# Optimization experiments

Hardware: AMD Instinct MI355X
Metric: run time of the kernel (lower is better)

## Reference

```python
import jax, jax.numpy as jnp
import numpy as np

NUM_HEADS = 16
LN_EPS = 1e-5

def _layernorm(x, g, b):
    m = jnp.mean(x, axis=-1, keepdims=True)
    v = jnp.var(x, axis=-1, keepdims=True)
    return (x - m) * jax.lax.rsqrt(v + LN_EPS) * g + b

def _mha(xq, xkv, qw, qb, kw, kb, vw, vb, ow, ob, causal):
    B, T, D = xq.shape
    S = xkv.shape[1]
    Hd = D // NUM_HEADS
    q = (xq @ qw + qb).reshape(B, T, NUM_HEADS, Hd)
    k = (xkv @ kw + kb).reshape(B, S, NUM_HEADS, Hd)
    v = (xkv @ vw + vb).reshape(B, S, NUM_HEADS, Hd)
    scores = jnp.einsum('bthd,bshd->bhts', q, k) / np.sqrt(Hd).astype(np.float32)
    if causal:
        mask = jnp.arange(T)[:, None] >= jnp.arange(S)[None, :]
        scores = jnp.where(mask, scores, jnp.float32(-jnp.inf))
    attn = jax.nn.softmax(scores, axis=-1)
    out = jnp.einsum('bhts,bshd->bthd', attn, v).reshape(B, T, D)
    return out @ ow + ob

def setup_inputs() -> dict:
    B, T, S, D, F = 4, 2048, 2048, 1024, 4096
    key = jax.random.key(0)
    ks = jax.random.split(key, 16)
    w = lambda k, shape: jax.random.normal(k, shape, dtype=jnp.float32) * 0.02
    z = lambda n: jnp.zeros((n,), jnp.float32)
    o = lambda n: jnp.ones((n,), jnp.float32)
    return {
        'x': jax.random.normal(ks[0], (B, T, D), dtype=jnp.float32),
        'encoder_output': jax.random.normal(ks[1], (B, S, D), dtype=jnp.float32),
        'sa_qw': w(ks[2], (D, D)), 'sa_qb': z(D),
        'sa_kw': w(ks[3], (D, D)), 'sa_kb': z(D),
        'sa_vw': w(ks[4], (D, D)), 'sa_vb': z(D),
        'sa_ow': w(ks[5], (D, D)), 'sa_ob': z(D),
        'ca_qw': w(ks[6], (D, D)), 'ca_qb': z(D),
        'ca_kw': w(ks[7], (D, D)), 'ca_kb': z(D),
        'ca_vw': w(ks[8], (D, D)), 'ca_vb': z(D),
        'ca_ow': w(ks[9], (D, D)), 'ca_ob': z(D),
        'ff_w1': w(ks[10], (D, F)), 'ff_b1': z(F),
        'ff_w2': w(ks[11], (F, D)), 'ff_b2': z(D),
        'ln1_g': o(D), 'ln1_b': z(D),
        'ln2_g': o(D), 'ln2_b': z(D),
        'ln3_g': o(D), 'ln3_b': z(D),
    }

def reference(x, encoder_output,
              sa_qw, sa_qb, sa_kw, sa_kb, sa_vw, sa_vb, sa_ow, sa_ob,
              ca_qw, ca_qb, ca_kw, ca_kb, ca_vw, ca_vb, ca_ow, ca_ob,
              ff_w1, ff_b1, ff_w2, ff_b2,
              ln1_g, ln1_b, ln2_g, ln2_b, ln3_g, ln3_b):
    # pre-norm causal self-attn + residual
    h = _layernorm(x, ln1_g, ln1_b)
    x = x + _mha(h, h, sa_qw, sa_qb, sa_kw, sa_kb, sa_vw, sa_vb, sa_ow, sa_ob, causal=True)
    # pre-norm cross-attn + residual
    h = _layernorm(x, ln2_g, ln2_b)
    x = x + _mha(h, encoder_output, ca_qw, ca_qb, ca_kw, ca_kb, ca_vw, ca_vb, ca_ow, ca_ob, causal=False)
    # pre-norm FFN + residual (dropout = identity in eval)
    h = _layernorm(x, ln3_g, ln3_b)
    x = x + (jax.nn.relu(h @ ff_w1 + ff_b1) @ ff_w2 + ff_b2)
    return x
```

## Files before the change

kernel.cpp:

```cpp
#include <hip/hip_runtime.h>
#include <stdint.h>

#define D_MODEL 1024
#define D_FF    4096
#define NHEADS  16
#define HD      64
#define LN_EPS  1e-5f

using u16 = unsigned short;
typedef __bf16 bf16x8 __attribute__((ext_vector_type(8)));
typedef float  f32x4  __attribute__((ext_vector_type(4)));
typedef float  f32x16 __attribute__((ext_vector_type(16)));

typedef __attribute__((address_space(1))) uint32_t as1_u32;
typedef __attribute__((address_space(3))) uint32_t as3_u32;

__device__ __forceinline__ u16 f2bf(float f) {
  union { float f; uint32_t u; } v; v.f = f;
  uint32_t r = v.u + 0x7FFFu + ((v.u >> 16) & 1u);
  return (u16)(r >> 16);
}

__device__ __forceinline__ uint32_t cvtpk(float lo, float hi) {
  uint32_t r;
  asm("v_cvt_pk_bf16_f32 %0, %1, %2" : "=v"(r) : "v"(lo), "v"(hi));
  return r;
}

__device__ __forceinline__ void gl_lds16(const void* g, void* l) {
  __builtin_amdgcn_global_load_lds((const as1_u32*)(uintptr_t)g,
                                   (as3_u32*)(uint32_t)(uintptr_t)l, 16, 0, 0);
}

__global__ __launch_bounds__(256)
void transpose_cast(const float* __restrict__ W, u16* __restrict__ Wt, int K, int N) {
  __shared__ float t[32][33];
  const int k0 = blockIdx.x * 32, n0 = blockIdx.y * 32;
  const int x = threadIdx.x & 31, y = threadIdx.x >> 5;
#pragma unroll
  for (int j = 0; j < 32; j += 8)
    t[y + j][x] = W[(size_t)(k0 + y + j) * N + (n0 + x)];
  __syncthreads();
#pragma unroll
  for (int j = 0; j < 32; j += 8)
    Wt[(size_t)(n0 + y + j) * K + (k0 + x)] = f2bf(t[x][y + j]);
}

struct Src8 { const float* s[8]; };
__global__ __launch_bounds__(256)
void transpose_cast8(Src8 p, u16* __restrict__ dstbase) {
  __shared__ float t[32][33];
  const float* __restrict__ W = p.s[blockIdx.z];
  u16* __restrict__ Wt = dstbase + (size_t)blockIdx.z * (1024 * 1024);
  const int k0 = blockIdx.x * 32, n0 = blockIdx.y * 32;
  const int x = threadIdx.x & 31, y = threadIdx.x >> 5;
#pragma unroll
  for (int j = 0; j < 32; j += 8)
    t[y + j][x] = W[(size_t)(k0 + y + j) * 1024 + (n0 + x)];
  __syncthreads();
#pragma unroll
  for (int j = 0; j < 32; j += 8)
    Wt[(size_t)(n0 + y + j) * 1024 + (k0 + x)] = f2bf(t[x][y + j]);
}

__global__ __launch_bounds__(256)
void cast_f32_bf16(const float* __restrict__ in, u16* __restrict__ out, int n4) {
  int i = blockIdx.x * 256 + threadIdx.x;
  if (i < n4) {
    float4 v = ((const float4*)in)[i];
    ushort4 o;
    o.x = f2bf(v.x); o.y = f2bf(v.y); o.z = f2bf(v.z); o.w = f2bf(v.w);
    ((ushort4*)out)[i] = o;
  }
}

__global__ __launch_bounds__(256)
void ln_bf16(const float* __restrict__ x, const float* __restrict__ g,
             const float* __restrict__ bta, u16* __restrict__ out) {
  const int row = blockIdx.x;
  const int tid = threadIdx.x;
  const float4 v = ((const float4*)(x + (size_t)row * D_MODEL))[tid];
  float s  = v.x + v.y + v.z + v.w;
  float s2 = v.x * v.x + v.y * v.y + v.z * v.z + v.w * v.w;
#pragma unroll
  for (int off = 1; off < 64; off <<= 1) {
    s  += __shfl_xor(s, off);
    s2 += __shfl_xor(s2, off);
  }
  __shared__ float sm[8];
  const int wave = tid >> 6, lane = tid & 63;
  if (lane == 0) { sm[wave] = s; sm[4 + wave] = s2; }
  __syncthreads();
  s  = sm[0] + sm[1] + sm[2] + sm[3];
  s2 = sm[4] + sm[5] + sm[6] + sm[7];
  const float mean = s * (1.f / D_MODEL);
  const float var  = s2 * (1.f / D_MODEL) - mean * mean;
  const float rstd = rsqrtf(var + LN_EPS);
  const float4 gv = ((const float4*)g)[tid];
  const float4 bv = ((const float4*)bta)[tid];
  ushort4 o;
  o.x = f2bf((v.x - mean) * rstd * gv.x + bv.x);
  o.y = f2bf((v.y - mean) * rstd * gv.y + bv.y);
  o.z = f2bf((v.z - mean) * rstd * gv.z + bv.z);
  o.w = f2bf((v.w - mean) * rstd * gv.w + bv.w);
  ((ushort4*)(out + (size_t)row * D_MODEL))[tid] = o;
}

#define QSCALE 0.18033688011112042f
template<int EPI>
__global__ __launch_bounds__(256, 3)
void gemm_bf16(const u16* __restrict__ A, const u16* __restrict__ Wt,
               const float* __restrict__ bias, const float* __restrict__ bias2,
               const float* __restrict__ bias3, const float* resid,
               u16* __restrict__ outb, u16* __restrict__ outb2, u16* __restrict__ outb3,
               float* outf, int M, int N, int K) {
  __shared__ u16 lA[128 * 32];
  __shared__ u16 lB[128 * 32];
  const int tid  = threadIdx.x;
  const int lane = tid & 63;
  const int wave = tid >> 6;
  const int wr = wave >> 1, wc = wave & 1;
  const int lr = lane & 15, lg = lane >> 4;
  const int row0 = blockIdx.x * 128, col0 = blockIdx.y * 128;

  const char* pa = (const char*)A  + ((size_t)(row0 + (tid >> 2)) * K + (size_t)(tid & 3) * 8) * 2;
  const char* pb = (const char*)Wt + ((size_t)(col0 + (tid >> 2)) * K + (size_t)(tid & 3) * 8) * 2;
  const size_t rowskip = (size_t)64 * K * 2;
  char* la = (char*)lA + wave * 1024;
  char* lb = (char*)lB + wave * 1024;

  f32x4 acc[4][4] = {};
  const int ksteps = K >> 5;
  for (int kt = 0; kt < ksteps; ++kt) {
    gl_lds16(pa, la);
    gl_lds16(pa + rowskip, la + 4096);
    gl_lds16(pb, lb);
    gl_lds16(pb + rowskip, lb + 4096);
    pa += 64; pb += 64;
    __syncthreads();
    bf16x8 af[4], bfr[4];
#pragma unroll
    for (int m = 0; m < 4; ++m)
      af[m] = *(const bf16x8*)((const char*)lA + (wr * 64 + m * 16 + lr) * 64 + lg * 16);
#pragma unroll
    for (int n = 0; n < 4; ++n)
      bfr[n] = *(const bf16x8*)((const char*)lB + (wc * 64 + n * 16 + lr) * 64 + lg * 16);
#pragma unroll
    for (int m = 0; m < 4; ++m)
#pragma unroll
      for (int n = 0; n < 4; ++n)
        acc[m][n] = __builtin_amdgcn_mfma_f32_16x16x32_bf16(af[m], bfr[n], acc[m][n], 0, 0, 0);
    __syncthreads();
  }

#pragma unroll
  for (int m = 0; m < 4; ++m) {
    const int grow = row0 + wr * 64 + m * 16 + lg * 4;
#pragma unroll
    for (int n = 0; n < 4; ++n) {
      const int gcol = col0 + wc * 64 + n * 16 + lr;
      float bv;
      float sc = 1.f;
      u16* optr = outb;
      if (EPI == 4) {
        const int seg = gcol >> 10;
        bv = ((seg == 0) ? bias : (seg == 1) ? bias2 : bias3)[gcol & 1023];
        optr = (seg == 0) ? outb : (seg == 1) ? outb2 : outb3;
        if (seg == 0) sc = QSCALE;
      } else if (EPI == 5) {
        const int seg = gcol >> 10;
        bv = (seg ? bias2 : bias)[gcol & 1023];
        optr = seg ? outb2 : outb;
      } else {
        bv = bias[gcol];
      }
#pragma unroll
      for (int r = 0; r < 4; ++r) {
        float v = acc[m][n][r] + bv;
        if (EPI == 0)      outb[(size_t)(grow + r) * N + gcol] = f2bf(v);
        else if (EPI == 1) outb[(size_t)(grow + r) * N + gcol] = f2bf(v > 0.f ? v : 0.f);
        else if (EPI == 3) outb[(size_t)(grow + r) * N + gcol] = f2bf(v * QSCALE);
        else if (EPI == 4 || EPI == 5)
          optr[(size_t)(grow + r) * 1024 + (gcol & 1023)] = f2bf(v * sc);
        else {
          const size_t idx = (size_t)(grow + r) * N + gcol;
          outf[idx] = v + resid[idx];
        }
      }
    }
  }
}

template<bool CAUSAL>
__global__ __launch_bounds__(256, 4)
void attn_kernel(const u16* __restrict__ Q, const u16* __restrict__ Kb,
                 const u16* __restrict__ Vb, u16* __restrict__ O,
                 int T, int S) {
  __shared__ u16 lQ[128 * 64];
  __shared__ u16 lK[64 * 64];
  __shared__ u16 lVt[64 * 64];

  const int f  = blockIdx.x;
  const int bh = f & 63;
  const int b = bh >> 4, hd = bh & 15;
  const int qx = f >> 6;
  const int q0 = (CAUSAL ? (T / 128 - 1 - qx) : qx) * 128;
  const int tid = threadIdx.x, lane = tid & 63, wave = tid >> 6;
  const int l31 = lane & 31, hb = lane >> 5;

  const u16* Qbase = Q  + (size_t)(b * T) * D_MODEL + hd * HD;
  const u16* Kbase = Kb + (size_t)(b * S) * D_MODEL + hd * HD;
  const u16* Vbase = Vb + (size_t)(b * S) * D_MODEL + hd * HD;
  const size_t rskip = (size_t)32 * D_MODEL * 2;

  const int srow = tid >> 3;
  const int sg   = (tid & 7) ^ (srow & 7);
  const int sprow = (srow & ~12) | ((srow & 4) << 1) | ((srow & 8) >> 1);

  {
    const char* src = (const char*)(Qbase + (size_t)(q0 + srow) * D_MODEL) + sg * 16;
    char* dst = (char*)lQ + wave * 1024;
    gl_lds16(src,             dst);
    gl_lds16(src + rskip,     dst + 4096);
    gl_lds16(src + 2 * rskip, dst + 8192);
    gl_lds16(src + 3 * rskip, dst + 12288);
  }

  bf16x8 qf[4];
  f32x16 oacc0 = {}, oacc1 = {};
  float m_run = -1e30f, l_run = 0.f;
  const int qq = q0 + wave * 32 + l31;

  const int ktEnd = CAUSAL ? (q0 / 64 + 2) : (S / 64);

  for (int kt = 0; kt < ktEnd; ++kt) {
    {
      const char* src = (const char*)(Kbase + (size_t)(kt * 64 + sprow) * D_MODEL) + sg * 16;
      char* dst = (char*)lK + wave * 1024;
      gl_lds16(src, dst);
      gl_lds16(src + rskip, dst + 4096);
    }
    {
      const u16* src = Vbase + (size_t)(kt * 64 + (tid >> 3)) * D_MODEL + (tid & 7) * 8;
      union { uint4 q; u16 s[8]; } v0, v1;
      v0.q = *(const uint4*)src;
      v1.q = *(const uint4*)(src + 32 * D_MODEL);
      const int key = tid >> 3, dbase = (tid & 7) * 8;
      const int kg0 = key >> 3, kb0 = (key & 7) * 2;
      const int kg1 = kg0 + 4;
#pragma unroll
      for (int j = 0; j < 8; ++j) {
        const int d = dbase + j;
        const int sw = (d >> 3) & 7;
        char* base = (char*)lVt + d * 128;
        *(u16*)(base + ((kg0 ^ sw) << 4) + kb0) = v0.s[j];
        *(u16*)(base + ((kg1 ^ sw) << 4) + kb0) = v1.s[j];
      }
    }
    __syncthreads();

    if (kt == 0) {
      const int qrow = wave * 32 + l31;
#pragma unroll
      for (int dc = 0; dc < 4; ++dc)
        qf[dc] = *(const bf16x8*)((const char*)lQ + qrow * 128 +
                                  (((2 * dc + hb) ^ (qrow & 7)) << 4));
    }

    const bool live = !CAUSAL || (kt * 64 <= q0 + wave * 32 + 31);
    if (live) {
      f32x16 z0 = {}, z1 = {};
      __builtin_amdgcn_s_setprio(1);
#pragma unroll
      for (int dc = 0; dc < 4; ++dc) {
        bf16x8 kf0 = *(const bf16x8*)((const char*)lK + l31 * 128 +
                                      (((2 * dc + hb) ^ (l31 & 7)) << 4));
        z0 = __builtin_amdgcn_mfma_f32_32x32x16_bf16(kf0, qf[dc], z0, 0, 0, 0);
      }
#pragma unroll
      for (int dc = 0; dc < 4; ++dc) {
        bf16x8 kf1 = *(const bf16x8*)((const char*)lK + (32 + l31) * 128 +
                                      (((2 * dc + hb) ^ (l31 & 7)) << 4));
        z1 = __builtin_amdgcn_mfma_f32_32x32x16_bf16(kf1, qf[dc], z1, 0, 0, 0);
      }
      __builtin_amdgcn_s_setprio(0);

      if (CAUSAL && kt * 64 + 63 > q0 + wave * 32) {
        const int kvb = kt * 64 + 8 * hb;
#pragma unroll
        for (int r = 0; r < 16; ++r) {
          const int kv = kvb + (r & 7) + 16 * (r >> 3);
          if (kv > qq)      z0[r] = -1e30f;
          if (kv + 32 > qq) z1[r] = -1e30f;
        }
      }

      float t[16];
#pragma unroll
      for (int r = 0; r < 16; ++r) t[r] = fmaxf(z0[r], z1[r]);
#pragma unroll
      for (int sdt = 8; sdt >= 1; sdt >>= 1)
#pragma unroll
        for (int i = 0; i < 8; ++i)
          if (i < sdt) t[i] = fmaxf(t[i], t[i + sdt]);
      float mx = t[0];
      mx = fmaxf(mx, __shfl_xor(mx, 32));

      if (!__all(mx - m_run <= 11.5f)) {
        const float mn = fmaxf(m_run, mx);
        const float scl = exp2f(m_run - mn);
        m_run = mn;
        l_run *= scl;
#pragma unroll
        for (int r = 0; r < 16; ++r) { oacc0[r] *= scl; oacc1[r] *= scl; }
      }
      float sum = 0.f;
#pragma unroll
      for (int r = 0; r < 16; ++r) {
        z0[r] = exp2f(z0[r] - m_run); sum += z0[r];
        z1[r] = exp2f(z1[r] - m_run); sum += z1[r];
      }
      sum += __shfl_xor(sum, 32);
      l_run += sum;

      bf16x8 pf[4];
      {
        union { uint32_t u[4]; bf16x8 v; } w0, w1, w2, w3;
#pragma unroll
        for (int i = 0; i < 4; ++i) {
          w0.u[i] = cvtpk(z0[2 * i],     z0[2 * i + 1]);
          w1.u[i] = cvtpk(z0[8 + 2 * i], z0[9 + 2 * i]);
          w2.u[i] = cvtpk(z1[2 * i],     z1[2 * i + 1]);
          w3.u[i] = cvtpk(z1[8 + 2 * i], z1[9 + 2 * i]);
        }
        pf[0] = w0.v; pf[1] = w1.v; pf[2] = w2.v; pf[3] = w3.v;
      }

      __builtin_amdgcn_s_setprio(1);
#pragma unroll
      for (int c = 0; c < 4; ++c) {
        bf16x8 vf0 = *(const bf16x8*)((const char*)lVt + l31 * 128 +
                       (((2 * c + hb) ^ ((l31 >> 3) & 7)) << 4));
        oacc0 = __builtin_amdgcn_mfma_f32_32x32x16_bf16(vf0, pf[c], oacc0, 0, 0, 0);
        bf16x8 vf1 = *(const bf16x8*)((const char*)lVt + (32 + l31) * 128 +
                       ((((2 * c + hb) ^ (((32 + l31) >> 3) & 7))) << 4));
        oacc1 = __builtin_amdgcn_mfma_f32_32x32x16_bf16(vf1, pf[c], oacc1, 0, 0, 0);
      }
      __builtin_amdgcn_s_setprio(0);
    }
    __syncthreads();
  }

  const float linv = 1.f / l_run;
  u16* Op = O + (size_t)(b * T + qq) * D_MODEL + hd * HD + 4 * hb;
#pragma unroll
  for (int rr = 0; rr < 4; ++rr) {
    uint2 st0, st1;
    st0.x = cvtpk(oacc0[4 * rr + 0] * linv, oacc0[4 * rr + 1] * linv);
    st0.y = cvtpk(oacc0[4 * rr + 2] * linv, oacc0[4 * rr + 3] * linv);
    *(uint2*)(Op + 8 * rr) = st0;
    st1.x = cvtpk(oacc1[4 * rr + 0] * linv, oacc1[4 * rr + 1] * linv);
    st1.y = cvtpk(oacc1[4 * rr + 2] * linv, oacc1[4 * rr + 3] * linv);
    *(uint2*)(Op + 32 + 8 * rr) = st1;
  }
}

extern "C" void kernel_launch(void* const* d_in, const int* in_sizes, int n_in,
                              void* d_out, int out_size, void* d_ws, size_t ws_size,
                              hipStream_t stream) {
  (void)in_sizes; (void)n_in; (void)out_size; (void)ws_size;
  const int B = 4, T = 2048, S = 2048, Dm = 1024, F = 4096;
  const int M = B * T;

  const float* x   = (const float*)d_in[0];
  const float* enc = (const float*)d_in[1];

  char* p = (char*)d_ws;
  auto take = [&](size_t bytes) { char* r = p; p += (bytes + 255) & ~(size_t)255; return r; };
  u16* wt8  = (u16*)take((size_t)8 * Dm * Dm * 2);
  u16* ff1T = (u16*)take((size_t)F * Dm * 2);
  u16* ff2T = (u16*)take((size_t)Dm * F * 2);
  u16*   h    = (u16*)take((size_t)M * Dm * 2);
  u16*   encb = (u16*)take((size_t)M * Dm * 2);
  float* xc   = (float*)take((size_t)M * Dm * 4);
  char*  Dreg = take((size_t)M * F * 2);
  u16* qb = (u16*)Dreg;
  u16* kb = (u16*)(Dreg + (size_t)M * Dm * 2);
  u16* vb = (u16*)(Dreg + (size_t)2 * M * Dm * 2);
  u16* ab = (u16*)(Dreg + (size_t)3 * M * Dm * 2);
  u16* ffmid = (u16*)Dreg;

  dim3 blk(256);
  Src8 s8 = {{ (const float*)d_in[2], (const float*)d_in[4], (const float*)d_in[6],
               (const float*)d_in[8], (const float*)d_in[10], (const float*)d_in[12],
               (const float*)d_in[14], (const float*)d_in[16] }};
  transpose_cast8<<<dim3(32, 32, 8), blk, 0, stream>>>(s8, wt8);
  transpose_cast<<<dim3(Dm / 32, F / 32), blk, 0, stream>>>((const float*)d_in[18], ff1T, Dm, F);
  transpose_cast<<<dim3(F / 32, Dm / 32), blk, 0, stream>>>((const float*)d_in[20], ff2T, F, Dm);
  cast_f32_bf16<<<dim3((M * Dm / 4) / 256), blk, 0, stream>>>(enc, encb, M * Dm / 4);

  dim3 gproj(M / 128, Dm / 128);
  dim3 gqkv(M / 128, 3072 / 128);
  dim3 gkv(M / 128, 2048 / 128);
  dim3 gffn1(M / 128, F / 128);
  dim3 gattn((T / 128) * 64);

  ln_bf16<<<M, blk, 0, stream>>>(x, (const float*)d_in[22], (const float*)d_in[23], h);
  gemm_bf16<4><<<gqkv, blk, 0, stream>>>(h, wt8,
      (const float*)d_in[3], (const float*)d_in[5], (const float*)d_in[7],
      nullptr, qb, kb, vb, nullptr, M, 3072, Dm);
  attn_kernel<true><<<gattn, blk, 0, stream>>>(qb, kb, vb, ab, T, S);
  gemm_bf16<2><<<gproj, blk, 0, stream>>>(ab, wt8 + (size_t)3 * Dm * Dm,
      (const float*)d_in[9], nullptr, nullptr, x, nullptr, nullptr, nullptr, xc, M, Dm, Dm);

  ln_bf16<<<M, blk, 0, stream>>>(xc, (const float*)d_in[24], (const float*)d_in[25], h);
  gemm_bf16<3><<<gproj, blk, 0, stream>>>(h, wt8 + (size_t)4 * Dm * Dm,
      (const float*)d_in[11], nullptr, nullptr, nullptr, qb, nullptr, nullptr, nullptr, M, Dm, Dm);
  gemm_bf16<5><<<gkv, blk, 0, stream>>>(encb, wt8 + (size_t)5 * Dm * Dm,
      (const float*)d_in[13], (const float*)d_in[15], nullptr,
      nullptr, kb, vb, nullptr, nullptr, M, 2048, Dm);
  attn_kernel<false><<<gattn, blk, 0, stream>>>(qb, kb, vb, ab, T, S);
  gemm_bf16<2><<<gproj, blk, 0, stream>>>(ab, wt8 + (size_t)7 * Dm * Dm,
      (const float*)d_in[17], nullptr, nullptr, xc, nullptr, nullptr, nullptr, xc, M, Dm, Dm);

  ln_bf16<<<M, blk, 0, stream>>>(xc, (const float*)d_in[26], (const float*)d_in[27], h);
  gemm_bf16<1><<<gffn1, blk, 0, stream>>>(h, ff1T, (const float*)d_in[19],
      nullptr, nullptr, nullptr, ffmid, nullptr, nullptr, nullptr, M, F, Dm);
  gemm_bf16<2><<<gproj, blk, 0, stream>>>(ffmid, ff2T, (const float*)d_in[21],
      nullptr, nullptr, xc, nullptr, nullptr, nullptr, (float*)d_out, M, Dm, F);
}
```

Measured before the change: 634.9 us.

## Write V transposed per head in QKV GEMM epilogue, load directly to LDS

```diff
diff --git a/kernel.cpp b/kernel.cpp
--- a/kernel.cpp
+++ b/kernel.cpp
@@ -159,32 +159,39 @@
 #pragma unroll
     for (int n = 0; n < 4; ++n) {
       const int gcol = col0 + wc * 64 + n * 16 + lr;
-      float bv;
-      float sc = 1.f;
-      u16* optr = outb;
-      if (EPI == 4) {
+      if (EPI == 4 || EPI == 5) {
         const int seg = gcol >> 10;
-        bv = ((seg == 0) ? bias : (seg == 1) ? bias2 : bias3)[gcol & 1023];
-        optr = (seg == 0) ? outb : (seg == 1) ? outb2 : outb3;
-        if (seg == 0) sc = QSCALE;
-      } else if (EPI == 5) {
-        const int seg = gcol >> 10;
-        bv = (seg ? bias2 : bias)[gcol & 1023];
-        optr = seg ? outb2 : outb;
+        const int c = gcol & 1023;
+        const bool isV = (EPI == 4) ? (seg == 2) : (seg == 1);
+        if (isV) {
+          const float bv = (EPI == 4 ? bias3 : bias2)[c];
+          const int hh = c >> 6, dd = c & 63;
+          const int bb = grow >> 11, tt = grow & 2047;
+          u16* vT = (EPI == 4) ? outb3 : outb2;
+          uint2 st;
+          st.x = cvtpk(acc[m][n][0] + bv, acc[m][n][1] + bv);
+          st.y = cvtpk(acc[m][n][2] + bv, acc[m][n][3] + bv);
+          *(uint2*)(vT + (((size_t)(bb * NHEADS + hh) * 64 + dd) << 11) + tt) = st;
+        } else {
+          const float bv = ((EPI == 4) ? ((seg == 0) ? bias : bias2) : bias)[c];
+          const float sc = (EPI == 4 && seg == 0) ? QSCALE : 1.f;
+          u16* optr = (EPI == 4) ? ((seg == 0) ? outb : outb2) : outb;
+#pragma unroll
+          for (int r = 0; r < 4; ++r)
+            optr[(size_t)(grow + r) * 1024 + c] = f2bf((acc[m][n][r] + bv) * sc);
+        }
       } else {
-        bv = bias[gcol];
-      }
-#pragma unroll
-      for (int r = 0; r < 4; ++r) {
-        float v = acc[m][n][r] + bv;
-        if (EPI == 0)      outb[(size_t)(grow + r) * N + gcol] = f2bf(v);
-        else if (EPI == 1) outb[(size_t)(grow + r) * N + gcol] = f2bf(v > 0.f ? v : 0.f);
-        else if (EPI == 3) outb[(size_t)(grow + r) * N + gcol] = f2bf(v * QSCALE);
-        else if (EPI == 4 || EPI == 5)
-          optr[(size_t)(grow + r) * 1024 + (gcol & 1023)] = f2bf(v * sc);
-        else {
-          const size_t idx = (size_t)(grow + r) * N + gcol;
-          outf[idx] = v + resid[idx];
+        const float bv = bias[gcol];
+#pragma unroll
+        for (int r = 0; r < 4; ++r) {
+          float v = acc[m][n][r] + bv;
+          if (EPI == 0)      outb[(size_t)(grow + r) * N + gcol] = f2bf(v);
+          else if (EPI == 1) outb[(size_t)(grow + r) * N + gcol] = f2bf(v > 0.f ? v : 0.f);
+          else if (EPI == 3) outb[(size_t)(grow + r) * N + gcol] = f2bf(v * QSCALE);
+          else {
+            const size_t idx = (size_t)(grow + r) * N + gcol;
+            outf[idx] = v + resid[idx];
+          }
         }
       }
     }
@@ -194,7 +201,7 @@
 template<bool CAUSAL>
 __global__ __launch_bounds__(256, 4)
 void attn_kernel(const u16* __restrict__ Q, const u16* __restrict__ Kb,
-                 const u16* __restrict__ Vb, u16* __restrict__ O,
+                 const u16* __restrict__ Vt, u16* __restrict__ O,
                  int T, int S) {
   __shared__ u16 lQ[128 * 64];
   __shared__ u16 lK[64 * 64];
@@ -210,11 +217,13 @@
 
   const u16* Qbase = Q  + (size_t)(b * T) * D_MODEL + hd * HD;
   const u16* Kbase = Kb + (size_t)(b * S) * D_MODEL + hd * HD;
-  const u16* Vbase = Vb + (size_t)(b * S) * D_MODEL + hd * HD;
+  const u16* Vbase = Vt + ((size_t)(b * NHEADS + hd) << 17);
   const size_t rskip = (size_t)32 * D_MODEL * 2;
 
   const int srow = tid >> 3;
   const int sg   = (tid & 7) ^ (srow & 7);
+  const int sgv0 = (tid & 7) ^ ((srow >> 3) & 7);
+  const int sgv1 = sgv0 ^ 4;
   const int sprow = (srow & ~12) | ((srow & 4) << 1) | ((srow & 8) >> 1);
 
   {
@@ -241,21 +250,10 @@
       gl_lds16(src + rskip, dst + 4096);
     }
     {
-      const u16* src = Vbase + (size_t)(kt * 64 + (tid >> 3)) * D_MODEL + (tid & 7) * 8;
-      union { uint4 q; u16 s[8]; } v0, v1;
-      v0.q = *(const uint4*)src;
-      v1.q = *(const uint4*)(src + 32 * D_MODEL);
-      const int key = tid >> 3, dbase = (tid & 7) * 8;
-      const int kg0 = key >> 3, kb0 = (key & 7) * 2;
-      const int kg1 = kg0 + 4;
-#pragma unroll
-      for (int j = 0; j < 8; ++j) {
-        const int d = dbase + j;
-        const int sw = (d >> 3) & 7;
-        char* base = (char*)lVt + d * 128;
-        *(u16*)(base + ((kg0 ^ sw) << 4) + kb0) = v0.s[j];
-        *(u16*)(base + ((kg1 ^ sw) << 4) + kb0) = v1.s[j];
-      }
+      const char* srcv = (const char*)(Vbase + ((size_t)srow << 11) + kt * 64);
+      char* dst = (char*)lVt + wave * 1024;
+      gl_lds16(srcv + sgv0 * 16, dst);
+      gl_lds16(srcv + (32u << 12) + sgv1 * 16, dst + 4096);
     }
     __syncthreads();
 
```

New measurement: 642.1 us. No clear change (+1.1%).
